# Kernel optimization log

Measured on AMD Instinct MI355X. Metric: run time of the kernel, lower is better.

The kernel has to match this reference:

```python
import jax, jax.numpy as jnp
import numpy as np

B, N, V, X, H, C = 128, 1023, 32000, 256, 256, 10  # N = 2^10 - 1 perfect binary tree (heap layout)


def setup_inputs() -> dict:
    key = jax.random.key(0)
    ks = jax.random.split(key, 12)
    s = 0.02
    return {
        "wordid": jax.random.randint(ks[0], (B, N), 0, V),
        "h0": jnp.zeros((B, N, H), jnp.float32),
        "c0": jnp.zeros((B, N, H), jnp.float32),
        "emb": jax.random.normal(ks[1], (V, X), jnp.float32) * s,
        "W_iou": jax.random.normal(ks[2], (3 * H, X), jnp.float32) * s,
        "U_iou": jax.random.normal(ks[3], (3 * H, 2 * H), jnp.float32) * s,
        "b_iou": jnp.zeros((1, 3 * H), jnp.float32),
        "Uf_W": jax.random.normal(ks[4], (2 * H, 2 * H), jnp.float32) * s,
        "Uf_b": jnp.zeros((2 * H,), jnp.float32),
        "Wmem": jax.random.normal(ks[5], (H, H), jnp.float32) * s,
        "wh_W": jax.random.normal(ks[6], (H, H), jnp.float32) * s,
        "wh_b": jnp.zeros((H,), jnp.float32),
        "lin_W": jax.random.normal(ks[7], (C, H), jnp.float32) * s,
        "lin_b": jnp.zeros((C,), jnp.float32),
    }


def _apply_node(iou, b_iou, c_in):
    # TreeLSTMCell.apply_node_func: iou -> i,o,u gates; c = sig(i)*tanh(u) + c_in; h = sig(o)*tanh(c)
    i, o, u = jnp.split(iou + b_iou, 3, axis=-1)
    c = jax.nn.sigmoid(i) * jnp.tanh(u) + c_in
    h = jax.nn.sigmoid(o) * jnp.tanh(c)
    return h, c


def reference(wordid, h0, c0, emb, W_iou, U_iou, b_iou, Uf_W, Uf_b, Wmem, wh_W, wh_b, lin_W, lin_b):
    Bn, Nn, Hn = h0.shape
    D = int(np.log2(Nn + 1))  # depth of perfect binary tree
    h, c = h0, c0
    # --- leaves (frontier 0): iou = W_iou(embed), c from initial state ---
    s = 2 ** (D - 1) - 1
    x_leaf = emb[wordid[:, s:]]                                  # [B, Nleaf, X]
    iou = jnp.einsum('bnx,gx->bng', x_leaf, W_iou)               # [B, Nleaf, 3H]
    hl, cl = _apply_node(iou, b_iou, c[:, s:])
    h = h.at[:, s:].set(hl)
    c = c.at[:, s:].set(cl)
    # --- internal levels, bottom-up (reduce_func overwrites iou and c) ---
    for level in range(D - 2, -1, -1):
        ps, pe = 2 ** level - 1, 2 ** (level + 1) - 1
        npar = pe - ps
        cs, ce = pe, pe + 2 * npar  # children of parent p live at 2p+1, 2p+2 (contiguous block)
        h_cat = h[:, cs:ce].reshape(Bn, npar, 2 * Hn)            # [B, npar, 2H]
        f = jax.nn.sigmoid(jnp.einsum('bnk,jk->bnj', h_cat, Uf_W) + Uf_b)
        f = f.reshape(Bn, npar, 2, Hn)
        c_sum = jnp.sum(f * c[:, cs:ce].reshape(Bn, npar, 2, Hn), axis=2)
        iou_p = jnp.einsum('bnk,gk->bng', h_cat, U_iou)          # [B, npar, 3H]
        hp, cp = _apply_node(iou_p, b_iou, c_sum)
        h = h.at[:, ps:pe].set(hp)
        c = c.at[:, ps:pe].set(cp)
    # --- TreeAttention: root (node 0 per tree) attends over all nodes of its tree ---
    dec = h[:, 0]                                                # [B, H]
    proj = jnp.einsum('bnh,gh->bng', h, Wmem)                    # memory_project
    scores = jnp.einsum('bh,bnh->bn', dec, proj)
    attn = jax.nn.softmax(scores, axis=1)                        # MaskedSoftmax, mask=None
    context = jnp.einsum('bn,bnh->bh', attn, h)                  # [B, H]
    hid = jax.nn.relu(context @ wh_W.T + wh_b)
    return hid @ lin_W.T + lin_b                                 # [B, num_classes]
```

## Files before the change

### kernel.cpp

```cpp
#include <hip/hip_runtime.h>
#include <math.h>

#define BB      128
#define NNODES  1023
#define HD      256
#define LEAVES  512
#define IOU3    768
#define CAT2    512
#define LDCOMB  1280

typedef unsigned short ushort_t;
typedef __bf16 bf16x8 __attribute__((ext_vector_type(8)));
typedef float  f32x4  __attribute__((ext_vector_type(4)));

__device__ __forceinline__ float sigf(float x) { return 1.0f / (1.0f + expf(-x)); }

__device__ __forceinline__ void gload16(const void* g, void* l)
{
    __builtin_amdgcn_global_load_lds(
        (const __attribute__((address_space(1))) unsigned int*)g,
        (__attribute__((address_space(3))) unsigned int*)l, 16, 0, 0);
}

__device__ __forceinline__ void split_bf16(float x, ushort_t& h, ushort_t& l)
{
    unsigned u = __float_as_uint(x);
    unsigned r = u + 0x7fff + ((u >> 16) & 1);
    h = (ushort_t)(r >> 16);
    float fh = __uint_as_float((unsigned)h << 16);
    float d = x - fh;
    unsigned u2 = __float_as_uint(d);
    unsigned r2 = u2 + 0x7fff + ((u2 >> 16) & 1);
    l = (ushort_t)(r2 >> 16);
}

__device__ __forceinline__ float rh2(ushort_t h, ushort_t l)
{
    return __uint_as_float((unsigned)h << 16) + __uint_as_float((unsigned)l << 16);
}

__global__ void k_split4(const float* __restrict__ src, ushort_t* __restrict__ hi,
                         ushort_t* __restrict__ lo, int n4)
{
    int i = blockIdx.x * 256 + threadIdx.x;
    if (i >= n4) return;
    float4 v = ((const float4*)src)[i];
    ushort4 hv, lv;
    split_bf16(v.x, hv.x, lv.x);
    split_bf16(v.y, hv.y, lv.y);
    split_bf16(v.z, hv.z, lv.z);
    split_bf16(v.w, hv.w, lv.w);
    ((ushort4*)hi)[i] = hv;
    ((ushort4*)lo)[i] = lv;
}

__global__ void k_build_wcat(const float* __restrict__ Uf, const float* __restrict__ Ui,
                             ushort_t* __restrict__ hi, ushort_t* __restrict__ lo)
{
    int i = blockIdx.x * 256 + threadIdx.x;
    if (i >= 1280 * 128) return;
    int row = i >> 7, c4 = i & 127;
    const float* src = (row < 512) ? (Uf + (size_t)row * 512)
                                   : (Ui + (size_t)(row - 512) * 512);
    float4 v = ((const float4*)src)[c4];
    ushort4 hv, lv;
    split_bf16(v.x, hv.x, lv.x);
    split_bf16(v.y, hv.y, lv.y);
    split_bf16(v.z, hv.z, lv.z);
    split_bf16(v.w, hv.w, lv.w);
    ((ushort4*)hi)[i] = hv;
    ((ushort4*)lo)[i] = lv;
}

#define BM 128
#define BN 128
#define BK 32

__global__ __launch_bounds__(256, 2)
void gemm_mfma(const ushort_t* __restrict__ Ahi, const ushort_t* __restrict__ Alo,
               const int* __restrict__ ids,
               int lognpar, unsigned sB, int sP, int m0, int K,
               const ushort_t* __restrict__ Bhi, const ushort_t* __restrict__ Blo,
               float* __restrict__ C, int ldc)
{
    __shared__ __align__(16) char lds[65536];
    const int tid = threadIdx.x;

    int bx = blockIdx.x, by = blockIdx.y;
    {
        const int gx = gridDim.x, gy = gridDim.y;
        if ((gx & 7) == 0) {
            int f = by * gx + bx;
            int span = gy << 3;
            int s = f / span;
            int wv = f - s * span;
            bx = (s << 3) + (wv & 7);
            by = wv >> 3;
        }
    }

    const int w = tid >> 6, lane = tid & 63;

    unsigned aofs[2], bofs[2];
    int dofs[2];
#pragma unroll
    for (int p = 0; p < 2; ++p) {
        int row = w * 32 + p * 16 + (lane >> 2);
        int slotp = (lane & 3) ^ ((row >> 1) & 3);
        int mg = m0 + bx * BM + row;
        unsigned ab;
        if (ids) {
            ab = (unsigned)ids[mg] * (unsigned)K;
        } else {
            int b = mg >> lognpar;
            int q = mg & ((1 << lognpar) - 1);
            ab = (unsigned)b * sB + (unsigned)q * (unsigned)sP;
        }
        aofs[p] = ab + slotp * 8;
        bofs[p] = (unsigned)(by * BN + row) * (unsigned)K + slotp * 8;
        dofs[p] = w * 2048 + p * 1024;
    }

    auto STAGE = [&](int k0, char* buf) {
#pragma unroll
        for (int p = 0; p < 2; ++p) {
            gload16(Ahi + aofs[p] + k0, buf +     0 + dofs[p]);
            gload16(Alo + aofs[p] + k0, buf +  8192 + dofs[p]);
            gload16(Bhi + bofs[p] + k0, buf + 16384 + dofs[p]);
            gload16(Blo + bofs[p] + k0, buf + 24576 + dofs[p]);
        }
    };

    const int wm = w >> 1, wn = w & 1;
    const int rA0 = wm * 64 + (lane & 15);
    const int rB0 = wn * 64 + (lane & 15);
    const int ko = lane >> 4;
    const int rdA = rA0 * 64 + ((ko ^ ((rA0 >> 1) & 3)) << 4);
    const int rdB = rB0 * 64 + ((ko ^ ((rB0 >> 1) & 3)) << 4);

    f32x4 acc[4][4];
#pragma unroll
    for (int mi = 0; mi < 4; ++mi)
#pragma unroll
        for (int ni = 0; ni < 4; ++ni) acc[mi][ni] = (f32x4){0.f, 0.f, 0.f, 0.f};

    const int nt = K / BK;
    STAGE(0, lds);
    int cur = 0;
    for (int t = 0; t < nt; ++t) {
        if (t + 1 < nt) {
            STAGE((t + 1) * BK, lds + (cur ^ 1) * 32768);
            asm volatile("s_waitcnt vmcnt(8)" ::: "memory");
        } else {
            asm volatile("s_waitcnt vmcnt(0)" ::: "memory");
        }
        __builtin_amdgcn_s_barrier();
        __builtin_amdgcn_sched_barrier(0);
        char* base = lds + cur * 32768;
        bf16x8 ah[4], al[4], bh[4], bl[4];
#pragma unroll
        for (int f = 0; f < 4; ++f) {
            ah[f] = *(const bf16x8*)(base +         rdA + f * 1024);
            al[f] = *(const bf16x8*)(base +  8192 + rdA + f * 1024);
            bh[f] = *(const bf16x8*)(base + 16384 + rdB + f * 1024);
            bl[f] = *(const bf16x8*)(base + 24576 + rdB + f * 1024);
        }
        __builtin_amdgcn_s_setprio(1);
#pragma unroll
        for (int mi = 0; mi < 4; ++mi)
#pragma unroll
            for (int ni = 0; ni < 4; ++ni) {
                acc[mi][ni] = __builtin_amdgcn_mfma_f32_16x16x32_bf16(ah[mi], bh[ni], acc[mi][ni], 0, 0, 0);
                acc[mi][ni] = __builtin_amdgcn_mfma_f32_16x16x32_bf16(ah[mi], bl[ni], acc[mi][ni], 0, 0, 0);
                acc[mi][ni] = __builtin_amdgcn_mfma_f32_16x16x32_bf16(al[mi], bh[ni], acc[mi][ni], 0, 0, 0);
            }
        __builtin_amdgcn_s_setprio(0);
        __builtin_amdgcn_s_barrier();
        cur ^= 1;
    }

    {
        char* patch = lds + w * 4352;
        const int cl = lane & 15, rg = lane >> 4;
        const int gcol0 = by * BN + wn * 64;
#pragma unroll
        for (int mi = 0; mi < 4; ++mi) {
#pragma unroll
            for (int ni = 0; ni < 4; ++ni)
#pragma unroll
                for (int r = 0; r < 4; ++r)
                    *(float*)(patch + (rg * 4 + r) * 272 + (ni * 16 + cl) * 4) = acc[mi][ni][r];
            int grow0 = bx * BM + wm * 64 + mi * 16;
#pragma unroll
            for (int it = 0; it < 4; ++it) {
                int lr = it * 4 + rg;
                f32x4 vv = *(const f32x4*)(patch + lr * 272 + cl * 16);
                *(f32x4*)(C + (size_t)(grow0 + lr) * ldc + gcol0 + cl * 4) = vv;
            }
        }
    }
}

__global__ void k_leaf_ids(const int* __restrict__ wordid, int* __restrict__ ids)
{
    int idx = blockIdx.x * 256 + threadIdx.x;
    int b = idx >> 9, leaf = idx & 511;
    ids[idx] = wordid[b * NNODES + 511 + leaf];
}

__global__ void k_apply_leaf(const float* __restrict__ buf, const float* __restrict__ b_iou,
                             const float* __restrict__ c0,
                             ushort_t* __restrict__ hhi, ushort_t* __restrict__ hlo,
                             float* __restrict__ c, int m0)
{
    int idx = blockIdx.x * 256 + threadIdx.x;
    int m_l = idx >> 8, hh = idx & 255;
    int mg = m0 + m_l;
    int b = mg >> 9, leaf = mg & 511;
    int node = 511 + leaf;
    const float* br = buf + (size_t)m_l * IOU3;
    float iv = br[hh]        + b_iou[hh];
    float ov = br[256 + hh]  + b_iou[256 + hh];
    float uv = br[512 + hh]  + b_iou[512 + hh];
    size_t nb = ((size_t)b * NNODES + node) * HD + hh;
    float cn = sigf(iv) * tanhf(uv) + c0[nb];
    float hn = sigf(ov) * tanhf(cn);
    c[nb] = cn;
    split_bf16(hn, hhi[nb], hlo[nb]);
}

__global__ void k_apply_level(const float* __restrict__ buf, const float* __restrict__ b_iou,
                              const float* __restrict__ Uf_b,
                              ushort_t* __restrict__ hhi, ushort_t* __restrict__ hlo,
                              float* __restrict__ c,
                              int m0, int lognpar, int ps, int cs)
{
    int idx = blockIdx.x * 256 + threadIdx.x;
    int m_l = idx >> 8, hh = idx & 255;
    int mg = m0 + m_l;
    int b = mg >> lognpar;
    int p = mg & ((1 << lognpar) - 1);
    const float* br = buf + (size_t)m_l * LDCOMB;
    float fl = sigf(br[hh]        + Uf_b[hh]);
    float fr = sigf(br[256 + hh]  + Uf_b[256 + hh]);
    size_t cb = ((size_t)b * NNODES + cs + 2 * p) * HD + hh;
    float csum = fl * c[cb] + fr * c[cb + HD];
    float iv = br[512 + hh]  + b_iou[hh];
    float ov = br[768 + hh]  + b_iou[256 + hh];
    float uv = br[1024 + hh] + b_iou[512 + hh];
    float cn = sigf(iv) * tanhf(uv) + csum;
    float hn = sigf(ov) * tanhf(cn);
    size_t pb = ((size_t)b * NNODES + ps + p) * HD + hh;
    c[pb] = cn;
    split_bf16(hn, hhi[pb], hlo[pb]);
}

__global__ void k_dec_v(const ushort_t* __restrict__ hhi, const ushort_t* __restrict__ hlo,
                        const float* __restrict__ Wmem, float* __restrict__ v)
{
    int b = blockIdx.x, k = threadIdx.x;
    __shared__ float dec[HD];
    size_t base = (size_t)b * NNODES * HD;
    dec[k] = rh2(hhi[base + k], hlo[base + k]);
    __syncthreads();
    float s = 0.f;
    for (int g = 0; g < HD; ++g) s = fmaf(dec[g], Wmem[g * HD + k], s);
    v[b * HD + k] = s;
}

__global__ void k_scores(const ushort_t* __restrict__ hhi, const ushort_t* __restrict__ hlo,
                         const float* __restrict__ v, float* __restrict__ scores)
{
    int b = blockIdx.x;
    int w = threadIdx.x >> 6, lane = threadIdx.x & 63;
    int n = blockIdx.y * 4 + w;
    if (n >= NNODES) return;
    size_t hb = ((size_t)b * NNODES + n) * HD;
    ushort4 ph = *(const ushort4*)(hhi + hb + lane * 4);
    ushort4 pl = *(const ushort4*)(hlo + hb + lane * 4);
    float4 vv = *(const float4*)(v + b * HD + lane * 4);
    float s = rh2(ph.x, pl.x) * vv.x + rh2(ph.y, pl.y) * vv.y +
              rh2(ph.z, pl.z) * vv.z + rh2(ph.w, pl.w) * vv.w;
#pragma unroll
    for (int o = 32; o; o >>= 1) s += __shfl_down(s, o);
    if (lane == 0) scores[(size_t)b * NNODES + n] = s;
}

__global__ void k_softmax(const float* __restrict__ scores, float* __restrict__ attn)
{
    int b = blockIdx.x, t = threadIdx.x;
    __shared__ float red[4];
    float sv[4];
    float m = -INFINITY;
#pragma unroll
    for (int i = 0; i < 4; ++i) {
        int n = t + 256 * i;
        sv[i] = (n < NNODES) ? scores[(size_t)b * NNODES + n] : -INFINITY;
        m = fmaxf(m, sv[i]);
    }
#pragma unroll
    for (int o = 32; o; o >>= 1) m = fmaxf(m, __shfl_xor(m, o));
    int w = t >> 6, lane = t & 63;
    if (lane == 0) red[w] = m;
    __syncthreads();
    m = fmaxf(fmaxf(red[0], red[1]), fmaxf(red[2], red[3]));
    float s = 0.f;
#pragma unroll
    for (int i = 0; i < 4; ++i) {
        int n = t + 256 * i;
        sv[i] = (n < NNODES) ? expf(sv[i] - m) : 0.f;
        s += sv[i];
    }
#pragma unroll
    for (int o = 32; o; o >>= 1) s += __shfl_xor(s, o);
    __syncthreads();
    if (lane == 0) red[w] = s;
    __syncthreads();
    s = red[0] + red[1] + red[2] + red[3];
    float inv = 1.0f / s;
#pragma unroll
    for (int i = 0; i < 4; ++i) {
        int n = t + 256 * i;
        if (n < NNODES) attn[(size_t)b * NNODES + n] = sv[i] * inv;
    }
}

__global__ void k_context(const ushort_t* __restrict__ hhi, const ushort_t* __restrict__ hlo,
                          const float* __restrict__ attn, float* __restrict__ partial)
{
    int b = blockIdx.x, ch = blockIdx.y, k = threadIdx.x;
    int n0 = ch * 128;
    int n1 = n0 + 128; if (n1 > NNODES) n1 = NNODES;
    float s = 0.f;
    for (int n = n0; n < n1; ++n) {
        size_t i = ((size_t)b * NNODES + n) * HD + k;
        s = fmaf(attn[(size_t)b * NNODES + n], rh2(hhi[i], hlo[i]), s);
    }
    partial[((size_t)b * 8 + ch) * HD + k] = s;
}

__global__ void k_final(const float* __restrict__ partial,
                        const float* __restrict__ wh_W, const float* __restrict__ wh_b,
                        const float* __restrict__ lin_W, const float* __restrict__ lin_b,
                        float* __restrict__ out)
{
    int b = blockIdx.x, j = threadIdx.x;
    __shared__ float ctx[HD];
    __shared__ float hid[HD];
    float s = 0.f;
#pragma unroll
    for (int ch = 0; ch < 8; ++ch) s += partial[((size_t)b * 8 + ch) * HD + j];
    ctx[j] = s;
    __syncthreads();
    float a = wh_b[j];
    for (int k = 0; k < HD; ++k) a = fmaf(ctx[k], wh_W[j * HD + k], a);
    hid[j] = fmaxf(a, 0.f);
    __syncthreads();
    if (j < 10) {
        float o = lin_b[j];
        for (int k = 0; k < HD; ++k) o = fmaf(hid[k], lin_W[j * HD + k], o);
        out[b * 10 + j] = o;
    }
}

extern "C" void kernel_launch(void* const* d_in, const int* in_sizes, int n_in,
                              void* d_out, int out_size, void* d_ws, size_t ws_size,
                              hipStream_t stream)
{
    const int*   wordid = (const int*)d_in[0];
    const float* c0     = (const float*)d_in[2];
    const float* emb    = (const float*)d_in[3];
    const float* W_iou  = (const float*)d_in[4];
    const float* U_iou  = (const float*)d_in[5];
    const float* b_iou  = (const float*)d_in[6];
    const float* Uf_W   = (const float*)d_in[7];
    const float* Uf_b   = (const float*)d_in[8];
    const float* Wmem   = (const float*)d_in[9];
    const float* wh_W   = (const float*)d_in[10];
    const float* wh_b   = (const float*)d_in[11];
    const float* lin_W  = (const float*)d_in[12];
    const float* lin_b  = (const float*)d_in[13];
    float* out = (float*)d_out;

    const int V = in_sizes[3] / 256;
    const size_t nh = (size_t)BB * NNODES * HD;

    char* ws = (char*)d_ws;
    size_t off = 0;
    auto alloc = [&](size_t bytes) -> void* {
        void* p = ws + off;
        off += (bytes + 255) & ~(size_t)255;
        return p;
    };
    ushort_t* hhi  = (ushort_t*)alloc(nh * 2);
    ushort_t* hlo  = (ushort_t*)alloc(nh * 2);
    float*    c    = (float*)   alloc(nh * 4);
    ushort_t* ehi  = (ushort_t*)alloc((size_t)V * 256 * 2);
    ushort_t* elo  = (ushort_t*)alloc((size_t)V * 256 * 2);
    ushort_t* wchi = (ushort_t*)alloc((size_t)LDCOMB * 512 * 2);
    ushort_t* wclo = (ushort_t*)alloc((size_t)LDCOMB * 512 * 2);
    ushort_t* wihi = (ushort_t*)alloc((size_t)IOU3 * 256 * 2);
    ushort_t* wilo = (ushort_t*)alloc((size_t)IOU3 * 256 * 2);
    int*   ids     = (int*)  alloc((size_t)BB * LEAVES * 4);
    float* v       = (float*)alloc((size_t)BB * HD * 4);
    float* scores  = (float*)alloc((size_t)BB * NNODES * 4);
    float* attn    = (float*)alloc((size_t)BB * NNODES * 4);
    float* partial = (float*)alloc((size_t)BB * 8 * HD * 4);

    size_t remain = (ws_size > off) ? (ws_size - off) : 0;
    size_t rows = remain / (LDCOMB * 4);
    int CH = (int)((rows > 16384) ? 16384 : rows);
    CH &= ~127;
    if (CH < 128) CH = 128;
    float* buf = (float*)alloc((size_t)CH * LDCOMB * 4);

    k_split4<<<(V * 256 / 4 + 255) / 256, 256, 0, stream>>>(emb, ehi, elo, V * 256 / 4);
    k_build_wcat<<<(1280 * 128 + 255) / 256, 256, 0, stream>>>(Uf_W, U_iou, wchi, wclo);
    k_split4<<<(IOU3 * 256 / 4 + 255) / 256, 256, 0, stream>>>(W_iou, wihi, wilo, IOU3 * 256 / 4);
    k_leaf_ids<<<(BB * LEAVES) / 256, 256, 0, stream>>>(wordid, ids);

    {
        int M = BB * LEAVES;
        for (int m0 = 0; m0 < M; m0 += CH) {
            int Mc = M - m0; if (Mc > CH) Mc = CH;
            dim3 g(Mc / BM, IOU3 / BN);
            gemm_mfma<<<g, 256, 0, stream>>>(ehi, elo, ids, 0, 0u, 0, m0, 256,
                                             wihi, wilo, buf, IOU3);
            k_apply_leaf<<<Mc, 256, 0, stream>>>(buf, b_iou, c0, hhi, hlo, c, m0);
        }
    }

    for (int L = 8; L >= 0; --L) {
        int npar = 1 << L;
        int ps = (1 << L) - 1;
        int cs = (1 << (L + 1)) - 1;
        int M = BB * npar;
        unsigned sB = NNODES * HD;
        int sP = 2 * HD;
        const ushort_t* Abh = hhi + (size_t)cs * HD;
        const ushort_t* Abl = hlo + (size_t)cs * HD;
        for (int m0 = 0; m0 < M; m0 += CH) {
            int Mc = M - m0; if (Mc > CH) Mc = CH;
            dim3 g(Mc / BM, LDCOMB / BN);
            gemm_mfma<<<g, 256, 0, stream>>>(Abh, Abl, (const int*)nullptr, L, sB, sP,
                                             m0, CAT2, wchi, wclo, buf, LDCOMB);
            k_apply_level<<<Mc, 256, 0, stream>>>(buf, b_iou, Uf_b, hhi, hlo, c,
                                                  m0, L, ps, cs);
        }
    }

    k_dec_v<<<BB, HD, 0, stream>>>(hhi, hlo, Wmem, v);
    k_scores<<<dim3(BB, 256), 256, 0, stream>>>(hhi, hlo, v, scores);
    k_softmax<<<BB, 256, 0, stream>>>(scores, attn);
    k_context<<<dim3(BB, 8), HD, 0, stream>>>(hhi, hlo, attn, partial);
    k_final<<<BB, HD, 0, stream>>>(partial, wh_W, wh_b, lin_W, lin_b, out);
}
```

Baseline: 777.4 us.

## Switch GEMM to 32x32x16 MFMA with BK=16 and higher occupancy

Rewrites the split-bf16 GEMM inner loop to use 32x32x16 MFMA tiles (2x2 per wave) instead of 16x16x32 (4x4), halving BK to 16. LDS use drops to 32KB, and launch bounds now target 4 blocks per CU so more waves can hide latency. The epilogue is reworked for the 32x32 accumulator layout. The leaf chunk size is also raised so fewer launches are needed. Risks are more barriers per K step with a shallower pipeline and possible register pressure at the higher occupancy target.

```diff
diff --git a/kernel.cpp b/kernel.cpp
--- a/kernel.cpp
+++ b/kernel.cpp
@@ -12,6 +12,7 @@
 typedef unsigned short ushort_t;
 typedef __bf16 bf16x8 __attribute__((ext_vector_type(8)));
 typedef float  f32x4  __attribute__((ext_vector_type(4)));
+typedef float  f32x16 __attribute__((ext_vector_type(16)));
 
 __device__ __forceinline__ float sigf(float x) { return 1.0f / (1.0f + expf(-x)); }
 
@@ -74,16 +75,16 @@
 
 #define BM 128
 #define BN 128
-#define BK 32
-
-__global__ __launch_bounds__(256, 2)
+#define BK 16
+
+__global__ __launch_bounds__(256, 4)
 void gemm_mfma(const ushort_t* __restrict__ Ahi, const ushort_t* __restrict__ Alo,
                const int* __restrict__ ids,
                int lognpar, unsigned sB, int sP, int m0, int K,
                const ushort_t* __restrict__ Bhi, const ushort_t* __restrict__ Blo,
                float* __restrict__ C, int ldc)
 {
-    __shared__ __align__(16) char lds[65536];
+    __shared__ __align__(16) char lds[32768];
     const int tid = threadIdx.x;
 
     int bx = blockIdx.x, by = blockIdx.y;
@@ -101,12 +102,10 @@
 
     const int w = tid >> 6, lane = tid & 63;
 
-    unsigned aofs[2], bofs[2];
-    int dofs[2];
-#pragma unroll
-    for (int p = 0; p < 2; ++p) {
-        int row = w * 32 + p * 16 + (lane >> 2);
-        int slotp = (lane & 3) ^ ((row >> 1) & 3);
+    unsigned aoff, boff;
+    {
+        int row = tid >> 1;
+        int hlog = (tid & 1) ^ ((row >> 2) & 1);
         int mg = m0 + bx * BM + row;
         unsigned ab;
         if (ids) {
@@ -116,63 +115,62 @@
             int q = mg & ((1 << lognpar) - 1);
             ab = (unsigned)b * sB + (unsigned)q * (unsigned)sP;
         }
-        aofs[p] = ab + slotp * 8;
-        bofs[p] = (unsigned)(by * BN + row) * (unsigned)K + slotp * 8;
-        dofs[p] = w * 2048 + p * 1024;
-    }
+        aoff = ab + hlog * 8;
+        boff = (unsigned)(by * BN + row) * (unsigned)K + hlog * 8;
+    }
+    const int wdst = w * 1024;
 
     auto STAGE = [&](int k0, char* buf) {
-#pragma unroll
-        for (int p = 0; p < 2; ++p) {
-            gload16(Ahi + aofs[p] + k0, buf +     0 + dofs[p]);
-            gload16(Alo + aofs[p] + k0, buf +  8192 + dofs[p]);
-            gload16(Bhi + bofs[p] + k0, buf + 16384 + dofs[p]);
-            gload16(Blo + bofs[p] + k0, buf + 24576 + dofs[p]);
-        }
+        gload16(Ahi + aoff + k0, buf +     0 + wdst);
+        gload16(Alo + aoff + k0, buf +  4096 + wdst);
+        gload16(Bhi + boff + k0, buf +  8192 + wdst);
+        gload16(Blo + boff + k0, buf + 12288 + wdst);
     };
 
     const int wm = w >> 1, wn = w & 1;
-    const int rA0 = wm * 64 + (lane & 15);
-    const int rB0 = wn * 64 + (lane & 15);
-    const int ko = lane >> 4;
-    const int rdA = rA0 * 64 + ((ko ^ ((rA0 >> 1) & 3)) << 4);
-    const int rdB = rB0 * 64 + ((ko ^ ((rB0 >> 1) & 3)) << 4);
-
-    f32x4 acc[4][4];
-#pragma unroll
-    for (int mi = 0; mi < 4; ++mi)
-#pragma unroll
-        for (int ni = 0; ni < 4; ++ni) acc[mi][ni] = (f32x4){0.f, 0.f, 0.f, 0.f};
+    const int frow = lane & 31, fh = lane >> 5;
+    const int arow0 = wm * 64 + frow;
+    const int brow0 = wn * 64 + frow;
+    const int rdA = (arow0 * 2 + (fh ^ ((arow0 >> 2) & 1))) * 16;
+    const int rdB = (brow0 * 2 + (fh ^ ((brow0 >> 2) & 1))) * 16;
+
+    f32x16 acc[2][2];
+#pragma unroll
+    for (int mi = 0; mi < 2; ++mi)
+#pragma unroll
+        for (int ni = 0; ni < 2; ++ni)
+#pragma unroll
+            for (int r = 0; r < 16; ++r) acc[mi][ni][r] = 0.f;
 
     const int nt = K / BK;
     STAGE(0, lds);
     int cur = 0;
     for (int t = 0; t < nt; ++t) {
         if (t + 1 < nt) {
-            STAGE((t + 1) * BK, lds + (cur ^ 1) * 32768);
-            asm volatile("s_waitcnt vmcnt(8)" ::: "memory");
+            STAGE((t + 1) * BK, lds + (cur ^ 1) * 16384);
+            asm volatile("s_waitcnt vmcnt(4)" ::: "memory");
         } else {
             asm volatile("s_waitcnt vmcnt(0)" ::: "memory");
         }
         __builtin_amdgcn_s_barrier();
         __builtin_amdgcn_sched_barrier(0);
-        char* base = lds + cur * 32768;
-        bf16x8 ah[4], al[4], bh[4], bl[4];
-#pragma unroll
-        for (int f = 0; f < 4; ++f) {
+        char* base = lds + cur * 16384;
+        bf16x8 ah[2], al[2], bh[2], bl[2];
+#pragma unroll
+        for (int f = 0; f < 2; ++f) {
             ah[f] = *(const bf16x8*)(base +         rdA + f * 1024);
-            al[f] = *(const bf16x8*)(base +  8192 + rdA + f * 1024);
-            bh[f] = *(const bf16x8*)(base + 16384 + rdB + f * 1024);
-            bl[f] = *(const bf16x8*)(base + 24576 + rdB + f * 1024);
+            al[f] = *(const bf16x8*)(base +  4096 + rdA + f * 1024);
+            bh[f] = *(const bf16x8*)(base +  8192 + rdB + f * 1024);
+            bl[f] = *(const bf16x8*)(base + 12288 + rdB + f * 1024);
         }
         __builtin_amdgcn_s_setprio(1);
 #pragma unroll
-        for (int mi = 0; mi < 4; ++mi)
-#pragma unroll
-            for (int ni = 0; ni < 4; ++ni) {
-                acc[mi][ni] = __builtin_amdgcn_mfma_f32_16x16x32_bf16(ah[mi], bh[ni], acc[mi][ni], 0, 0, 0);
-                acc[mi][ni] = __builtin_amdgcn_mfma_f32_16x16x32_bf16(ah[mi], bl[ni], acc[mi][ni], 0, 0, 0);
-                acc[mi][ni] = __builtin_amdgcn_mfma_f32_16x16x32_bf16(al[mi], bh[ni], acc[mi][ni], 0, 0, 0);
+        for (int mi = 0; mi < 2; ++mi)
+#pragma unroll
+            for (int ni = 0; ni < 2; ++ni) {
+                acc[mi][ni] = __builtin_amdgcn_mfma_f32_32x32x16_bf16(ah[mi], bh[ni], acc[mi][ni], 0, 0, 0);
+                acc[mi][ni] = __builtin_amdgcn_mfma_f32_32x32x16_bf16(ah[mi], bl[ni], acc[mi][ni], 0, 0, 0);
+                acc[mi][ni] = __builtin_amdgcn_mfma_f32_32x32x16_bf16(al[mi], bh[ni], acc[mi][ni], 0, 0, 0);
             }
         __builtin_amdgcn_s_setprio(0);
         __builtin_amdgcn_s_barrier();
@@ -183,19 +181,26 @@
         char* patch = lds + w * 4352;
         const int cl = lane & 15, rg = lane >> 4;
         const int gcol0 = by * BN + wn * 64;
-#pragma unroll
-        for (int mi = 0; mi < 4; ++mi) {
-#pragma unroll
-            for (int ni = 0; ni < 4; ++ni)
-#pragma unroll
-                for (int r = 0; r < 4; ++r)
-                    *(float*)(patch + (rg * 4 + r) * 272 + (ni * 16 + cl) * 4) = acc[mi][ni][r];
-            int grow0 = bx * BM + wm * 64 + mi * 16;
-#pragma unroll
-            for (int it = 0; it < 4; ++it) {
-                int lr = it * 4 + rg;
-                f32x4 vv = *(const f32x4*)(patch + lr * 272 + cl * 16);
-                *(f32x4*)(C + (size_t)(grow0 + lr) * ldc + gcol0 + cl * 4) = vv;
+        const int prow4 = 4 * fh;
+#pragma unroll
+        for (int mi = 0; mi < 2; ++mi) {
+#pragma unroll
+            for (int hf = 0; hf < 2; ++hf) {
+#pragma unroll
+                for (int ni = 0; ni < 2; ++ni)
+#pragma unroll
+                    for (int rr = 0; rr < 8; ++rr) {
+                        int r = hf * 8 + rr;
+                        int prow = (rr & 3) + 8 * ((rr >> 2) & 1) + prow4;
+                        *(float*)(patch + prow * 272 + (ni * 32 + frow) * 4) = acc[mi][ni][r];
+                    }
+                int grow0 = bx * BM + wm * 64 + mi * 32 + hf * 16;
+#pragma unroll
+                for (int it = 0; it < 4; ++it) {
+                    int lr = it * 4 + rg;
+                    f32x4 vv = *(const f32x4*)(patch + lr * 272 + cl * 16);
+                    *(f32x4*)(C + (size_t)(grow0 + lr) * ldc + gcol0 + cl * 4) = vv;
+                }
             }
         }
     }
@@ -409,7 +414,7 @@
 
     size_t remain = (ws_size > off) ? (ws_size - off) : 0;
     size_t rows = remain / (LDCOMB * 4);
-    int CH = (int)((rows > 16384) ? 16384 : rows);
+    int CH = (int)((rows > 32768) ? 32768 : rows);
     CH &= ~127;
     if (CH < 128) CH = 128;
     float* buf = (float*)alloc((size_t)CH * LDCOMB * 4);
```

New measurement: 888.1 us. 14.2% more time.
